# Optimization experiments

Hardware: AMD Instinct MI355X
Metric: run time of the kernel (lower is better)

Reference implementation:

```python
import jax, jax.numpy as jnp
import numpy as np

B, N, C_IN, HID, K, DEG = 8192, 64, 128, 128, 5, 8


def setup_inputs() -> dict:
    key = jax.random.key(0)
    ks = jax.random.split(key, 8)
    total = B * N
    E = B * N * DEG
    x = jax.random.normal(ks[0], (total, C_IN), dtype=jnp.float32)
    batch = jnp.repeat(jnp.arange(B, dtype=jnp.int64), N)
    g = jnp.repeat(jnp.arange(B, dtype=jnp.int64), N * DEG)
    src = g * N + jax.random.randint(ks[1], (E,), 0, N).astype(jnp.int64)
    dst = g * N + jax.random.randint(ks[2], (E,), 0, N).astype(jnp.int64)
    edge_index = jnp.stack([src, dst])  # [2, E]
    s = 0.05
    return {
        "x": x,
        "edge_index": edge_index,
        "batch": batch,
        "W_pool": jax.random.normal(ks[3], (C_IN, K), dtype=jnp.float32) * s,
        "b_pool": jnp.zeros((K,), jnp.float32),
        "W1": jax.random.normal(ks[4], (C_IN, HID), dtype=jnp.float32) * s,
        "b1": jnp.zeros((HID,), jnp.float32),
        "W2": jax.random.normal(ks[5], (HID, HID), dtype=jnp.float32) * s,
        "b2": jnp.zeros((HID,), jnp.float32),
        "W_lin": jax.random.normal(ks[6], (HID, 1), dtype=jnp.float32) * s,
        "b_lin": jnp.zeros((1,), jnp.float32),
        "num_graphs": B,
        "max_nodes": N,
    }


def dense_gcn(x, adj, W, b, mask=None):
    # PyG DenseGCNConv with add_loop=True: diagonal set to 1 on a copy
    n = adj.shape[1]
    idx = jnp.arange(n)
    adj_l = adj.at[:, idx, idx].set(1.0)
    out = x @ W  # [B, n, out]
    d = jnp.clip(adj_l.sum(-1), 1.0) ** -0.5  # [B, n]
    adj_n = d[:, :, None] * adj_l * d[:, None, :]
    out = jnp.einsum('bnm,bmc->bnc', adj_n, out) + b
    if mask is not None:
        out = out * mask[..., None]
    return out


def reference(x, edge_index, batch, W_pool, b_pool, W1, b1, W2, b2, W_lin, b_lin,
              num_graphs, max_nodes):
    total = x.shape[0]
    # to_dense_batch: position of each node within its graph (batch is sorted)
    first_idx = jax.ops.segment_min(jnp.arange(total), batch, num_segments=num_graphs)
    pos = jnp.arange(total) - first_idx[batch]
    x_dense = jnp.zeros((num_graphs, max_nodes, x.shape[1]), x.dtype).at[batch, pos].set(x)
    mask = jnp.zeros((num_graphs, max_nodes), x.dtype).at[batch, pos].set(1.0)
    # to_dense_adj
    src, dst = edge_index[0], edge_index[1]
    adj = jnp.zeros((num_graphs, max_nodes, max_nodes), x.dtype)
    adj = adj.at[batch[src], pos[src], pos[dst]].add(1.0)

    s = dense_gcn(x_dense, adj, W_pool, b_pool, mask)       # [B, N, K]
    x_l1 = dense_gcn(x_dense, adj, W1, b1, mask)            # [B, N, H]

    # dense_diff_pool (losses are discarded by the original forward)
    s = jax.nn.softmax(s, axis=-1) * mask[..., None]
    xm = x_l1 * mask[..., None]
    x_p1 = jnp.einsum('bnk,bnc->bkc', s, xm)                # [B, K, H]
    adj_p1 = jnp.einsum('bnk,bnm,bml->bkl', s, adj, s)      # [B, K, K]

    x_l2 = dense_gcn(x_p1, adj_p1, W2, b2)                  # [B, K, H]
    pooled = x_l2.sum(axis=1)                               # global_add_pool -> [B, H]
    return pooled @ W_lin + b_lin                           # [B, 1]
```

## Files before the change

### kernel.cpp

```cpp
#include <hip/hip_runtime.h>
#include <hip/hip_bf16.h>

#define NN 64
#define CI 128
#define HD 128
#define KC 5
#define SXS 136
#define AJW 17

#define WS_Y   1024
#define WS_B1Z 1152
#define WS_B2W 1153

typedef float v4f __attribute__((ext_vector_type(4)));
typedef __bf16 v8bf __attribute__((ext_vector_type(8)));
typedef unsigned short us8 __attribute__((ext_vector_type(8)));

__device__ __forceinline__ unsigned short f2us(float f) {
    __hip_bfloat16 h = __float2bfloat16(f);
    return *reinterpret_cast<unsigned short*>(&h);
}

extern "C" __global__ void zprep(const float* __restrict__ W1,
                                 const float* __restrict__ Wp,
                                 const float* __restrict__ W2,
                                 const float* __restrict__ Wl,
                                 const float* __restrict__ b1,
                                 const float* __restrict__ b2,
                                 float* __restrict__ ws)
{
    const int b = blockIdx.x, t = threadIdx.x;
    if (b < 4) {
        const int ks = b;
        const int q = t >> 4, m16 = t & 15;
        const int k0 = ks * 32 + q * 8;
        us8 pk;
        #pragma unroll
        for (int j = 0; j < 8; ++j) {
            const int k = k0 + j;
            pk[j] = f2us((m16 < KC) ? Wp[k * KC + m16] : 0.f);
        }
        reinterpret_cast<us8*>(ws)[b * 64 + t] = pk;
    } else {
        __shared__ float sz_[HD];
        float a0 = 0.f, a1 = 0.f;
        for (int c = 0; c < HD; ++c) {
            const float wl = Wl[c];
            a0 += W2[t * HD + c] * wl;
            a1 += W2[(t + 64) * HD + c] * wl;
        }
        sz_[t] = a0; sz_[t + 64] = a1;
        float p1 = b1[t] * a0 + b1[t + 64] * a1;
        float p2 = b2[t] * Wl[t] + b2[t + 64] * Wl[t + 64];
        #pragma unroll
        for (int off = 32; off; off >>= 1) {
            p1 += __shfl_down(p1, off, 64);
            p2 += __shfl_down(p2, off, 64);
        }
        if (t == 0) { ws[WS_B1Z] = p1; ws[WS_B2W] = p2; }
        __syncthreads();
        #pragma unroll
        for (int rr = 0; rr < 2; ++rr) {
            const int r = t + rr * 64;
            float acc = 0.f;
            for (int h2 = 0; h2 < HD; ++h2) acc += W1[r * HD + h2] * sz_[h2];
            ws[WS_Y + r] = acc;
        }
    }
}

extern "C" __global__ __launch_bounds__(256, 6)
void diffpool_main(const float* __restrict__ x,
                   const int* __restrict__ ei,
                   const float* __restrict__ bp,
                   const float* __restrict__ bl,
                   const float* __restrict__ ws,
                   float* __restrict__ out,
                   int E, int epg)
{
    __shared__ __attribute__((aligned(16))) union {
        unsigned short sx[NN][SXS];
        struct {
            float A[4][NN * KC];
            float Bu[4][NN * KC];
            float pp[4][25];
        } s;
    } u;
    __shared__ unsigned int sadjb[NN][AJW];
    __shared__ float sSm[NN][KC];
    __shared__ float sq[NN];
    __shared__ float sd[NN];
    __shared__ float sw_[NN];
    __shared__ unsigned int srdeg[NN];
    __shared__ float sadjp[25];
    __shared__ float sd2[KC];
    __shared__ float scoef[KC];

    const int t = threadIdx.x;
    const int g = blockIdx.x;
    const int lane = t & 63;
    const int wv = t >> 6;
    const int n = lane;
    const int h = wv;

    const float bp0 = bp[0], bp1 = bp[1], bp2 = bp[2], bp3 = bp[3], bp4 = bp[4];
    const float c_b1z = ws[WS_B1Z], c_b2w = ws[WS_B2W], c_bl = bl[0];

    const int ch = t & 15;
    const float4 y0 = *reinterpret_cast<const float4*>(ws + WS_Y + ch * 8);
    const float4 y1 = *reinterpret_cast<const float4*>(ws + WS_Y + ch * 8 + 4);

    int e0s = -1, e0d = 0, e1s = -1, e1d = 0;
    const int base = g * epg;
    if (t < epg)       { e0s = ei[base + t] & 63;        e0d = ei[E + base + t] & 63; }
    if (t + 256 < epg) { e1s = ei[base + t + 256] & 63;  e1d = ei[E + base + t + 256] & 63; }

    {
        unsigned int* ap = &sadjb[0][0];
        for (int i = t; i < NN * AJW; i += 256) ap[i] = 0u;
        if (t < NN) srdeg[t] = 0u;
        const float* xg = x + (size_t)g * (NN * CI);
        #pragma unroll
        for (int i = 0; i < 4; ++i) {
            const int row = (t >> 4) + 16 * i;
            const float4 v0 = *reinterpret_cast<const float4*>(xg + row * CI + ch * 8);
            const float4 v1 = *reinterpret_cast<const float4*>(xg + row * CI + ch * 8 + 4);
            us8 pk;
            pk[0] = f2us(v0.x); pk[1] = f2us(v0.y); pk[2] = f2us(v0.z); pk[3] = f2us(v0.w);
            pk[4] = f2us(v1.x); pk[5] = f2us(v1.y); pk[6] = f2us(v1.z); pk[7] = f2us(v1.w);
            *reinterpret_cast<us8*>(&u.sx[row][ch * 8]) = pk;
            float qp = v0.x * y0.x + v0.y * y0.y + v0.z * y0.z + v0.w * y0.w
                     + v1.x * y1.x + v1.y * y1.y + v1.z * y1.z + v1.w * y1.w;
            qp += __shfl_down(qp, 8, 16);
            qp += __shfl_down(qp, 4, 16);
            qp += __shfl_down(qp, 2, 16);
            qp += __shfl_down(qp, 1, 16);
            if (ch == 0) sq[row] = qp;
        }
    }
    __syncthreads();

    {
        if (e0s >= 0) {
            atomicAdd(&sadjb[e0s][e0d >> 2], 1u << ((e0d & 3) * 8));
            atomicAdd(&srdeg[e0s], 1u);
        }
        if (e1s >= 0) {
            atomicAdd(&sadjb[e1s][e1d >> 2], 1u << ((e1d & 3) * 8));
            atomicAdd(&srdeg[e1s], 1u);
        }
        for (int j = t + 512; j < epg; j += 256) {
            const int sn = ei[base + j] & 63;
            const int dn = ei[E + base + j] & 63;
            atomicAdd(&sadjb[sn][dn >> 2], 1u << ((dn & 3) * 8));
            atomicAdd(&srdeg[sn], 1u);
        }
    }
    {
        const int m16 = lane & 15;
        const int q = lane >> 4;
        const int arow = wv * 16 + m16;
        const v8bf* wpk = reinterpret_cast<const v8bf*>(ws);
        v4f acc = {0.f, 0.f, 0.f, 0.f};
        #pragma unroll
        for (int ks = 0; ks < 4; ++ks) {
            const v8bf afrag = *reinterpret_cast<const v8bf*>(&u.sx[arow][ks * 32 + q * 8]);
            acc = __builtin_amdgcn_mfma_f32_16x16x32_bf16(afrag, wpk[ks * 64 + lane], acc, 0, 0, 0);
        }
        if (m16 < KC) {
            #pragma unroll
            for (int r = 0; r < 4; ++r)
                sSm[wv * 16 + q * 4 + r][m16] = acc[r];
        }
    }
    __syncthreads();

    unsigned aw0, aw1, aw2, aw3;
    float dlane;
    {
        const unsigned selfb = (sadjb[lane][lane >> 2] >> ((lane & 3) * 8)) & 255u;
        dlane = rsqrtf((float)(srdeg[lane] + 1u - selfb));
        sd[lane] = dlane;
        aw0 = sadjb[n][h * 4 + 0];
        aw1 = sadjb[n][h * 4 + 1];
        aw2 = sadjb[n][h * 4 + 2];
        aw3 = sadjb[n][h * 4 + 3];
        float a0 = 0.f, a1 = 0.f, a2 = 0.f, a3 = 0.f, a4 = 0.f;
        #pragma unroll
        for (int i = 0; i < 4; ++i) {
            const unsigned w = (i == 0) ? aw0 : (i == 1) ? aw1 : (i == 2) ? aw2 : aw3;
            #pragma unroll
            for (int bb = 0; bb < 4; ++bb) {
                const int m = h * 16 + i * 4 + bb;
                const float al = (m == n) ? 1.f : (float)((w >> (bb * 8)) & 255u);
                const float f = al * sd[m];
                a0 += f * sSm[m][0]; a1 += f * sSm[m][1]; a2 += f * sSm[m][2];
                a3 += f * sSm[m][3]; a4 += f * sSm[m][4];
            }
        }
        float* pp = &u.s.A[h][n * KC];
        pp[0] = a0; pp[1] = a1; pp[2] = a2; pp[3] = a3; pp[4] = a4;
    }
    __syncthreads();

    float s0v, s1v, s2v, s3v, s4v;
    {
        float a0 = u.s.A[0][n*KC+0] + u.s.A[1][n*KC+0] + u.s.A[2][n*KC+0] + u.s.A[3][n*KC+0];
        float a1 = u.s.A[0][n*KC+1] + u.s.A[1][n*KC+1] + u.s.A[2][n*KC+1] + u.s.A[3][n*KC+1];
        float a2 = u.s.A[0][n*KC+2] + u.s.A[1][n*KC+2] + u.s.A[2][n*KC+2] + u.s.A[3][n*KC+2];
        float a3 = u.s.A[0][n*KC+3] + u.s.A[1][n*KC+3] + u.s.A[2][n*KC+3] + u.s.A[3][n*KC+3];
        float a4 = u.s.A[0][n*KC+4] + u.s.A[1][n*KC+4] + u.s.A[2][n*KC+4] + u.s.A[3][n*KC+4];
        a0 = a0 * dlane + bp0; a1 = a1 * dlane + bp1; a2 = a2 * dlane + bp2;
        a3 = a3 * dlane + bp3; a4 = a4 * dlane + bp4;
        const float mx = fmaxf(fmaxf(fmaxf(a0, a1), fmaxf(a2, a3)), a4);
        a0 = expf(a0 - mx); a1 = expf(a1 - mx); a2 = expf(a2 - mx);
        a3 = expf(a3 - mx); a4 = expf(a4 - mx);
        const float inv = 1.f / (a0 + a1 + a2 + a3 + a4);
        s0v = a0 * inv; s1v = a1 * inv; s2v = a2 * inv; s3v = a3 * inv; s4v = a4 * inv;
        sSm[n][0] = s0v; sSm[n][1] = s1v; sSm[n][2] = s2v;
        sSm[n][3] = s3v; sSm[n][4] = s4v;
        float u0 = 0.f, u1 = 0.f, u2 = 0.f, u3 = 0.f, u4 = 0.f;
        #pragma unroll
        for (int i = 0; i < 4; ++i) {
            const unsigned w = (i == 0) ? aw0 : (i == 1) ? aw1 : (i == 2) ? aw2 : aw3;
            #pragma unroll
            for (int bb = 0; bb < 4; ++bb) {
                const int m = h * 16 + i * 4 + bb;
                const float c = (float)((w >> (bb * 8)) & 255u);
                u0 += c * sSm[m][0]; u1 += c * sSm[m][1]; u2 += c * sSm[m][2];
                u3 += c * sSm[m][3]; u4 += c * sSm[m][4];
            }
        }
        float* pp = &u.s.Bu[h][n * KC];
        pp[0] = u0; pp[1] = u1; pp[2] = u2; pp[3] = u3; pp[4] = u4;
    }
    __syncthreads();

    if (lane < 25) {
        const int k = lane / 5, l = lane - k * 5;
        float a = 0.f;
        #pragma unroll
        for (int i = 0; i < 16; ++i) {
            const int m = h * 16 + i;
            const float uu = u.s.Bu[0][m*KC+l] + u.s.Bu[1][m*KC+l]
                           + u.s.Bu[2][m*KC+l] + u.s.Bu[3][m*KC+l];
            a += sSm[m][k] * uu;
        }
        u.s.pp[h][lane] = a;
    }
    __syncthreads();

    float cbv;
    {
        if (lane < 25)
            sadjp[lane] = u.s.pp[0][lane] + u.s.pp[1][lane] + u.s.pp[2][lane] + u.s.pp[3][lane];
        if (lane < KC) {
            float s_ = 0.f;
            #pragma unroll
            for (int l = 0; l < KC; ++l) s_ += sadjp[lane * KC + l];
            s_ += 1.f - sadjp[lane * 6];
            sd2[lane] = rsqrtf(fmaxf(s_, 1.f));
        }
        if (lane < KC) {
            float a = 0.f;
            #pragma unroll
            for (int k = 0; k < KC; ++k) a += sd2[k] * sadjp[k * KC + lane];
            a += sd2[lane] * (1.f - sadjp[lane * 6]);
            scoef[lane] = sd2[lane] * a;
        }
        float t5 = scoef[0] * s0v + scoef[1] * s1v + scoef[2] * s2v +
                   scoef[3] * s3v + scoef[4] * s4v;
        sw_[n] = dlane * t5;
        cbv = t5;
        #pragma unroll
        for (int off = 32; off; off >>= 1) cbv += __shfl_down(cbv, off, 64);
        float pa = 0.f;
        #pragma unroll
        for (int i = 0; i < 16; ++i) {
            const int nn2 = h * 16 + i;
            const float al = (nn2 == n) ? 1.f
                           : (float)((sadjb[nn2][n >> 2] >> ((n & 3) * 8)) & 255u);
            pa += sw_[nn2] * al;
        }
        u.s.A[h][n] = pa;
    }
    __syncthreads();

    if (wv == 0) {
        const float a = u.s.A[0][n] + u.s.A[1][n] + u.s.A[2][n] + u.s.A[3][n];
        float v = dlane * a * sq[n];
        #pragma unroll
        for (int off = 32; off; off >>= 1) v += __shfl_down(v, off, 64);
        if (lane == 0)
            out[g] = v + cbv * c_b1z + 5.f * c_b2w + c_bl;
    }
}

extern "C" void kernel_launch(void* const* d_in, const int* in_sizes, int n_in,
                              void* d_out, int out_size, void* d_ws, size_t ws_size,
                              hipStream_t stream) {
    const float* x  = (const float*)d_in[0];
    const int*   ei = (const int*)d_in[1];
    const float* Wp = (const float*)d_in[3];
    const float* bp = (const float*)d_in[4];
    const float* W1 = (const float*)d_in[5];
    const float* b1 = (const float*)d_in[6];
    const float* W2 = (const float*)d_in[7];
    const float* b2 = (const float*)d_in[8];
    const float* Wl = (const float*)d_in[9];
    const float* bl = (const float*)d_in[10];
    float* out = (float*)d_out;
    float* ws  = (float*)d_ws;

    const int B = out_size;
    const int E = in_sizes[1] / 2;
    const int epg = E / B;

    zprep<<<5, 64, 0, stream>>>(W1, Wp, W2, Wl, b1, b2, ws);
    diffpool_main<<<B, 256, 0, stream>>>(x, ei, bp, bl, ws, out, E, epg);
}
```

Measured before the change: 423.6 us.

## Load x directly into MFMA fragments, drop LDS staging, fold final pass

The main kernel no longer stages x as bf16 in shared memory. Each lane reads its own row slice from global memory, converts it to bf16 in registers and feeds the MFMA directly, computing the q dot product in the same loop. The last adjacency pass is replaced by a precomputed per-node term (A_hat·q) built during the first aggregation, which removes one barrier and one shared-memory pass. This also shrinks LDS so the launch bound can rise to 8 blocks, and zprep is merged into a single block. The trade-off is global loads that are less coalesced, since each lane reads 32-byte pieces spread across rows, and zprep now does all its work serially in one block.

```diff
diff --git a/kernel.cpp b/kernel.cpp
--- a/kernel.cpp
+++ b/kernel.cpp
@@ -5,7 +5,6 @@
 #define CI 128
 #define HD 128
 #define KC 5
-#define SXS 136
 #define AJW 17
 
 #define WS_Y   1024
@@ -29,47 +28,44 @@
                                  const float* __restrict__ b2,
                                  float* __restrict__ ws)
 {
-    const int b = blockIdx.x, t = threadIdx.x;
-    if (b < 4) {
-        const int ks = b;
-        const int q = t >> 4, m16 = t & 15;
+    const int t = threadIdx.x;
+    __shared__ float sz_[HD];
+    float a0 = 0.f, a1 = 0.f;
+    for (int c = 0; c < HD; ++c) {
+        const float wl = Wl[c];
+        a0 += W2[t * HD + c] * wl;
+        a1 += W2[(t + 64) * HD + c] * wl;
+    }
+    sz_[t] = a0; sz_[t + 64] = a1;
+    float p1 = b1[t] * a0 + b1[t + 64] * a1;
+    float p2 = b2[t] * Wl[t] + b2[t + 64] * Wl[t + 64];
+    #pragma unroll
+    for (int off = 32; off; off >>= 1) {
+        p1 += __shfl_down(p1, off, 64);
+        p2 += __shfl_down(p2, off, 64);
+    }
+    if (t == 0) { ws[WS_B1Z] = p1; ws[WS_B2W] = p2; }
+    __syncthreads();
+    #pragma unroll
+    for (int rr = 0; rr < 2; ++rr) {
+        const int r = t + rr * 64;
+        float acc = 0.f;
+        for (int h2 = 0; h2 < HD; ++h2) acc += W1[r * HD + h2] * sz_[h2];
+        ws[WS_Y + r] = acc;
+    }
+    const int q = t >> 4, m16 = t & 15;
+    #pragma unroll
+    for (int ks = 0; ks < 4; ++ks) {
         const int k0 = ks * 32 + q * 8;
         us8 pk;
         #pragma unroll
-        for (int j = 0; j < 8; ++j) {
-            const int k = k0 + j;
-            pk[j] = f2us((m16 < KC) ? Wp[k * KC + m16] : 0.f);
-        }
-        reinterpret_cast<us8*>(ws)[b * 64 + t] = pk;
-    } else {
-        __shared__ float sz_[HD];
-        float a0 = 0.f, a1 = 0.f;
-        for (int c = 0; c < HD; ++c) {
-            const float wl = Wl[c];
-            a0 += W2[t * HD + c] * wl;
-            a1 += W2[(t + 64) * HD + c] * wl;
-        }
-        sz_[t] = a0; sz_[t + 64] = a1;
-        float p1 = b1[t] * a0 + b1[t + 64] * a1;
-        float p2 = b2[t] * Wl[t] + b2[t + 64] * Wl[t + 64];
-        #pragma unroll
-        for (int off = 32; off; off >>= 1) {
-            p1 += __shfl_down(p1, off, 64);
-            p2 += __shfl_down(p2, off, 64);
-        }
-        if (t == 0) { ws[WS_B1Z] = p1; ws[WS_B2W] = p2; }
-        __syncthreads();
-        #pragma unroll
-        for (int rr = 0; rr < 2; ++rr) {
-            const int r = t + rr * 64;
-            float acc = 0.f;
-            for (int h2 = 0; h2 < HD; ++h2) acc += W1[r * HD + h2] * sz_[h2];
-            ws[WS_Y + r] = acc;
-        }
-    }
-}
-
-extern "C" __global__ __launch_bounds__(256, 6)
+        for (int j = 0; j < 8; ++j)
+            pk[j] = f2us((m16 < KC) ? Wp[(k0 + j) * KC + m16] : 0.f);
+        reinterpret_cast<us8*>(ws)[ks * 64 + t] = pk;
+    }
+}
+
+extern "C" __global__ __launch_bounds__(256, 8)
 void diffpool_main(const float* __restrict__ x,
                    const int* __restrict__ ei,
                    const float* __restrict__ bp,
@@ -78,20 +74,16 @@
                    float* __restrict__ out,
                    int E, int epg)
 {
-    __shared__ __attribute__((aligned(16))) union {
-        unsigned short sx[NN][SXS];
-        struct {
-            float A[4][NN * KC];
-            float Bu[4][NN * KC];
-            float pp[4][25];
-        } s;
-    } u;
     __shared__ unsigned int sadjb[NN][AJW];
+    __shared__ float sA [4][NN * KC];
+    __shared__ float sBu[4][NN * KC];
+    __shared__ float sc [4][NN];
+    __shared__ float spp[4][25];
     __shared__ float sSm[NN][KC];
     __shared__ float sq[NN];
     __shared__ float sd[NN];
-    __shared__ float sw_[NN];
     __shared__ unsigned int srdeg[NN];
+    __shared__ float sz_[HD];
     __shared__ float sadjp[25];
     __shared__ float sd2[KC];
     __shared__ float scoef[KC];
@@ -100,15 +92,14 @@
     const int g = blockIdx.x;
     const int lane = t & 63;
     const int wv = t >> 6;
+    const int q4 = lane >> 4;
+    const int m16 = lane & 15;
     const int n = lane;
     const int h = wv;
+    const int arow = wv * 16 + m16;
 
     const float bp0 = bp[0], bp1 = bp[1], bp2 = bp[2], bp3 = bp[3], bp4 = bp[4];
     const float c_b1z = ws[WS_B1Z], c_b2w = ws[WS_B2W], c_bl = bl[0];
-
-    const int ch = t & 15;
-    const float4 y0 = *reinterpret_cast<const float4*>(ws + WS_Y + ch * 8);
-    const float4 y1 = *reinterpret_cast<const float4*>(ws + WS_Y + ch * 8 + 4);
 
     int e0s = -1, e0d = 0, e1s = -1, e1d = 0;
     const int base = g * epg;
@@ -119,24 +110,8 @@
         unsigned int* ap = &sadjb[0][0];
         for (int i = t; i < NN * AJW; i += 256) ap[i] = 0u;
         if (t < NN) srdeg[t] = 0u;
-        const float* xg = x + (size_t)g * (NN * CI);
-        #pragma unroll
-        for (int i = 0; i < 4; ++i) {
-            const int row = (t >> 4) + 16 * i;
-            const float4 v0 = *reinterpret_cast<const float4*>(xg + row * CI + ch * 8);
-            const float4 v1 = *reinterpret_cast<const float4*>(xg + row * CI + ch * 8 + 4);
-            us8 pk;
-            pk[0] = f2us(v0.x); pk[1] = f2us(v0.y); pk[2] = f2us(v0.z); pk[3] = f2us(v0.w);
-            pk[4] = f2us(v1.x); pk[5] = f2us(v1.y); pk[6] = f2us(v1.z); pk[7] = f2us(v1.w);
-            *reinterpret_cast<us8*>(&u.sx[row][ch * 8]) = pk;
-            float qp = v0.x * y0.x + v0.y * y0.y + v0.z * y0.z + v0.w * y0.w
-                     + v1.x * y1.x + v1.y * y1.y + v1.z * y1.z + v1.w * y1.w;
-            qp += __shfl_down(qp, 8, 16);
-            qp += __shfl_down(qp, 4, 16);
-            qp += __shfl_down(qp, 2, 16);
-            qp += __shfl_down(qp, 1, 16);
-            if (ch == 0) sq[row] = qp;
-        }
+        if (t < 32)
+            reinterpret_cast<float4*>(sz_)[t] = reinterpret_cast<const float4*>(ws + WS_Y)[t];
     }
     __syncthreads();
 
@@ -157,20 +132,32 @@
         }
     }
     {
-        const int m16 = lane & 15;
-        const int q = lane >> 4;
-        const int arow = wv * 16 + m16;
+        const float* xr = x + (size_t)g * (NN * CI) + arow * CI;
         const v8bf* wpk = reinterpret_cast<const v8bf*>(ws);
         v4f acc = {0.f, 0.f, 0.f, 0.f};
+        float qp = 0.f;
         #pragma unroll
         for (int ks = 0; ks < 4; ++ks) {
-            const v8bf afrag = *reinterpret_cast<const v8bf*>(&u.sx[arow][ks * 32 + q * 8]);
-            acc = __builtin_amdgcn_mfma_f32_16x16x32_bf16(afrag, wpk[ks * 64 + lane], acc, 0, 0, 0);
-        }
+            const int c0 = ks * 32 + q4 * 8;
+            const float4 v0 = *reinterpret_cast<const float4*>(xr + c0);
+            const float4 v1 = *reinterpret_cast<const float4*>(xr + c0 + 4);
+            const float4 y0 = *reinterpret_cast<const float4*>(sz_ + c0);
+            const float4 y1 = *reinterpret_cast<const float4*>(sz_ + c0 + 4);
+            qp += v0.x * y0.x + v0.y * y0.y + v0.z * y0.z + v0.w * y0.w
+                + v1.x * y1.x + v1.y * y1.y + v1.z * y1.z + v1.w * y1.w;
+            us8 pk;
+            pk[0] = f2us(v0.x); pk[1] = f2us(v0.y); pk[2] = f2us(v0.z); pk[3] = f2us(v0.w);
+            pk[4] = f2us(v1.x); pk[5] = f2us(v1.y); pk[6] = f2us(v1.z); pk[7] = f2us(v1.w);
+            const v8bf af = *reinterpret_cast<const v8bf*>(&pk);
+            acc = __builtin_amdgcn_mfma_f32_16x16x32_bf16(af, wpk[ks * 64 + lane], acc, 0, 0, 0);
+        }
+        qp += __shfl_xor(qp, 16, 64);
+        qp += __shfl_xor(qp, 32, 64);
+        if (q4 == 0) sq[arow] = qp;
         if (m16 < KC) {
             #pragma unroll
             for (int r = 0; r < 4; ++r)
-                sSm[wv * 16 + q * 4 + r][m16] = acc[r];
+                sSm[wv * 16 + q4 * 4 + r][m16] = acc[r];
         }
     }
     __syncthreads();
@@ -185,7 +172,7 @@
         aw1 = sadjb[n][h * 4 + 1];
         aw2 = sadjb[n][h * 4 + 2];
         aw3 = sadjb[n][h * 4 + 3];
-        float a0 = 0.f, a1 = 0.f, a2 = 0.f, a3 = 0.f, a4 = 0.f;
+        float a0 = 0.f, a1 = 0.f, a2 = 0.f, a3 = 0.f, a4 = 0.f, cp = 0.f;
         #pragma unroll
         for (int i = 0; i < 4; ++i) {
             const unsigned w = (i == 0) ? aw0 : (i == 1) ? aw1 : (i == 2) ? aw2 : aw3;
@@ -196,20 +183,22 @@
                 const float f = al * sd[m];
                 a0 += f * sSm[m][0]; a1 += f * sSm[m][1]; a2 += f * sSm[m][2];
                 a3 += f * sSm[m][3]; a4 += f * sSm[m][4];
+                cp += f * sq[m];
             }
         }
-        float* pp = &u.s.A[h][n * KC];
+        float* pp = &sA[h][n * KC];
         pp[0] = a0; pp[1] = a1; pp[2] = a2; pp[3] = a3; pp[4] = a4;
+        sc[h][n] = cp;
     }
     __syncthreads();
 
     float s0v, s1v, s2v, s3v, s4v;
     {
-        float a0 = u.s.A[0][n*KC+0] + u.s.A[1][n*KC+0] + u.s.A[2][n*KC+0] + u.s.A[3][n*KC+0];
-        float a1 = u.s.A[0][n*KC+1] + u.s.A[1][n*KC+1] + u.s.A[2][n*KC+1] + u.s.A[3][n*KC+1];
-        float a2 = u.s.A[0][n*KC+2] + u.s.A[1][n*KC+2] + u.s.A[2][n*KC+2] + u.s.A[3][n*KC+2];
-        float a3 = u.s.A[0][n*KC+3] + u.s.A[1][n*KC+3] + u.s.A[2][n*KC+3] + u.s.A[3][n*KC+3];
-        float a4 = u.s.A[0][n*KC+4] + u.s.A[1][n*KC+4] + u.s.A[2][n*KC+4] + u.s.A[3][n*KC+4];
+        float a0 = sA[0][n*KC+0] + sA[1][n*KC+0] + sA[2][n*KC+0] + sA[3][n*KC+0];
+        float a1 = sA[0][n*KC+1] + sA[1][n*KC+1] + sA[2][n*KC+1] + sA[3][n*KC+1];
+        float a2 = sA[0][n*KC+2] + sA[1][n*KC+2] + sA[2][n*KC+2] + sA[3][n*KC+2];
+        float a3 = sA[0][n*KC+3] + sA[1][n*KC+3] + sA[2][n*KC+3] + sA[3][n*KC+3];
+        float a4 = sA[0][n*KC+4] + sA[1][n*KC+4] + sA[2][n*KC+4] + sA[3][n*KC+4];
         a0 = a0 * dlane + bp0; a1 = a1 * dlane + bp1; a2 = a2 * dlane + bp2;
         a3 = a3 * dlane + bp3; a4 = a4 * dlane + bp4;
         const float mx = fmaxf(fmaxf(fmaxf(a0, a1), fmaxf(a2, a3)), a4);
@@ -231,7 +220,7 @@
                 u3 += c * sSm[m][3]; u4 += c * sSm[m][4];
             }
         }
-        float* pp = &u.s.Bu[h][n * KC];
+        float* pp = &sBu[h][n * KC];
         pp[0] = u0; pp[1] = u1; pp[2] = u2; pp[3] = u3; pp[4] = u4;
     }
     __syncthreads();
@@ -242,18 +231,17 @@
         #pragma unroll
         for (int i = 0; i < 16; ++i) {
             const int m = h * 16 + i;
-            const float uu = u.s.Bu[0][m*KC+l] + u.s.Bu[1][m*KC+l]
-                           + u.s.Bu[2][m*KC+l] + u.s.Bu[3][m*KC+l];
+            const float uu = sBu[0][m*KC+l] + sBu[1][m*KC+l]
+                           + sBu[2][m*KC+l] + sBu[3][m*KC+l];
             a += sSm[m][k] * uu;
         }
-        u.s.pp[h][lane] = a;
-    }
-    __syncthreads();
-
-    float cbv;
+        spp[h][lane] = a;
+    }
+    __syncthreads();
+
     {
         if (lane < 25)
-            sadjp[lane] = u.s.pp[0][lane] + u.s.pp[1][lane] + u.s.pp[2][lane] + u.s.pp[3][lane];
+            sadjp[lane] = spp[0][lane] + spp[1][lane] + spp[2][lane] + spp[3][lane];
         if (lane < KC) {
             float s_ = 0.f;
             #pragma unroll
@@ -268,31 +256,19 @@
             a += sd2[lane] * (1.f - sadjp[lane * 6]);
             scoef[lane] = sd2[lane] * a;
         }
-        float t5 = scoef[0] * s0v + scoef[1] * s1v + scoef[2] * s2v +
-                   scoef[3] * s3v + scoef[4] * s4v;
-        sw_[n] = dlane * t5;
-        cbv = t5;
-        #pragma unroll
-        for (int off = 32; off; off >>= 1) cbv += __shfl_down(cbv, off, 64);
-        float pa = 0.f;
-        #pragma unroll
-        for (int i = 0; i < 16; ++i) {
-            const int nn2 = h * 16 + i;
-            const float al = (nn2 == n) ? 1.f
-                           : (float)((sadjb[nn2][n >> 2] >> ((n & 3) * 8)) & 255u);
-            pa += sw_[nn2] * al;
-        }
-        u.s.A[h][n] = pa;
-    }
-    __syncthreads();
-
-    if (wv == 0) {
-        const float a = u.s.A[0][n] + u.s.A[1][n] + u.s.A[2][n] + u.s.A[3][n];
-        float v = dlane * a * sq[n];
-        #pragma unroll
-        for (int off = 32; off; off >>= 1) v += __shfl_down(v, off, 64);
-        if (lane == 0)
-            out[g] = v + cbv * c_b1z + 5.f * c_b2w + c_bl;
+        const float t5 = scoef[0] * s0v + scoef[1] * s1v + scoef[2] * s2v +
+                         scoef[3] * s3v + scoef[4] * s4v;
+        const float wn = dlane * t5;
+        const float cfull = sc[0][n] + sc[1][n] + sc[2][n] + sc[3][n];
+        float cb = t5;
+        float v = wn * cfull;
+        #pragma unroll
+        for (int off = 32; off; off >>= 1) {
+            cb += __shfl_down(cb, off, 64);
+            v  += __shfl_down(v,  off, 64);
+        }
+        if (wv == 0 && lane == 0)
+            out[g] = v + cb * c_b1z + 5.f * c_b2w + c_bl;
     }
 }
 
@@ -316,6 +292,6 @@
     const int E = in_sizes[1] / 2;
     const int epg = E / B;
 
-    zprep<<<5, 64, 0, stream>>>(W1, Wp, W2, Wl, b1, b2, ws);
+    zprep<<<1, 64, 0, stream>>>(W1, Wp, W2, Wl, b1, b2, ws);
     diffpool_main<<<B, 256, 0, stream>>>(x, ei, bp, bl, ws, out, E, epg);
 }
```

Result: slower. 453.4 us (+7.0%).
